# Optimization experiments

Hardware: AMD Instinct MI355X
Metric: run time of the kernel (lower is better)

Reference implementation:

```python
import jax, jax.numpy as jnp
import numpy as np

BNUM, BNOD = 4, 8
NODE_NUM = BNUM * BNUM * BNOD  # 128
EPS = 1e-9


def setup_inputs() -> dict:
    key = jax.random.key(0)
    k1, k2, k3 = jax.random.split(key, 3)
    x = jax.random.normal(k1, (8, 512, 64, 64), dtype=jnp.float32)
    anchor = jax.random.uniform(k2, (NODE_NUM, 512), dtype=jnp.float32)
    sigma = jax.random.uniform(k3, (NODE_NUM, 512), dtype=jnp.float32)
    return {"x": x, "anchor": anchor, "sigma": sigma}


def reference(x, anchor, sigma):
    B, C, H, W = x.shape
    h, w = H // BNUM, W // BNUM
    n = h * w                       # pixels per spatial block
    G = BNUM * BNUM                 # number of spatial blocks
    # Gather all spatial blocks at once: (B,C,H,W) -> (B, G, n, C)
    blocks = x.reshape(B, C, BNUM, h, BNUM, w)
    blocks = blocks.transpose(0, 2, 4, 3, 5, 1).reshape(B, G, n, C)
    a = anchor.reshape(G, BNOD, C)
    s = sigma.reshape(G, BNOD, C)
    # Gaussian residual per (block, node, pixel): (B, G, BNOD, n, C)
    resid = (blocks[:, :, None, :, :] - a[None, :, :, None, :]) / s[None, :, :, None, :]
    # -||residual||^2 / 2 over channels -> (B, G, BNOD, n)
    logits = -0.5 * jnp.sum(resid * resid, axis=-1)
    # Block-wise softmax over the BNOD nodes of each block
    soft = jax.nn.softmax(logits, axis=2)
    # Soft-assignment-weighted mean residual per node: (B, G, BNOD, C)
    nodes = jnp.einsum('bgknc,bgkn->bgkc', resid, soft)
    nodes = nodes / (jnp.sum(soft, axis=3)[..., None] + EPS)
    # Intra-node L2 normalization over channels (F.normalize, dim=2)
    norm = jnp.linalg.norm(nodes, axis=-1, keepdims=True)
    nodes = nodes / jnp.maximum(norm, 1e-12)
    nodes = nodes.reshape(B, NODE_NUM, C).transpose(0, 2, 1)   # (B, C, node_num)
    soft_assign = soft.reshape(B, NODE_NUM, n)                 # (B, node_num, n)
    return nodes, soft_assign
```

## Files before the change

kernel.cpp:

```cpp
#include <hip/hip_runtime.h>


#define NCH 512

typedef __attribute__((address_space(3))) void lds_void_t;
typedef const __attribute__((address_space(1))) void gbl_void_t;

__device__ __forceinline__ void gload_lds16(const float* g, float* l) {
  __builtin_amdgcn_global_load_lds((gbl_void_t*)g, (lds_void_t*)l, 16, 0, 0);
}

struct SharedMain {
  float anc[NCH * 16];
  float chunk[NCH * 16];
  float scratch[8 * 16 * 8];
  float soft[16 * 8];
};

__global__ __launch_bounds__(512, 4)
void gp_main(const float* __restrict__ x,
             const float* __restrict__ anchor,
             const float* __restrict__ sigma,
             float* __restrict__ soft_out,
             float* __restrict__ ws_s1,
             int parts_log2) {
  __shared__ SharedMain sh;
  const int tid = threadIdx.x;

  const int qb   = blockIdx.x;
  const int xcd  = qb & 7;
  const int slot = qb >> 3;
  const int gx   = slot & 3;
  const int Gp   = slot >> 2;
  const int G    = Gp * 8 + xcd;
  const int gy   = G & 3;
  const int tG   = G >> 2;
  const int parts = 1 << parts_log2;
  const int part  = tG & (parts - 1);
  const int b     = tG >> parts_log2;
  const int g     = gy * 4 + gx;
  const int nrows = 16 >> parts_log2;
  const int y0    = gy * 16 + part * nrows;
  const int x0    = gx * 16;
  const float* xb = x + (size_t)b * (NCH * 4096);

  {
    const float* ab = anchor + g * (8 * NCH);
    const float* sb = sigma  + g * (8 * NCH);
#pragma unroll
    for (int e = 0; e < 8; ++e) {
      int idx = e * 512 + tid;
      int k   = idx >> 9;
      int ci  = idx & 511;
      float a = ab[idx];
      float r = 1.0f / sb[idx];
      int sw  = (ci >> 4) & 3;
      int fq0 = (k >> 2) ^ sw;
      int fq1 = (2 + (k >> 2)) ^ sw;
      sh.anc[ci * 16 + (fq0 << 2) + (k & 3)] = r;
      sh.anc[ci * 16 + (fq1 << 2) + (k & 3)] = a * r;
    }
  }

  float S1[8];
#pragma unroll
  for (int k = 0; k < 8; ++k) S1[k] = 0.0f;

  const int cg   = tid >> 4;
  const int p    = tid & 15;
  const int wv   = tid >> 6;
  const int lane = tid & 63;
  const int asw  = cg & 3;

  for (int cc = 0; cc < nrows; ++cc) {
    const int y = y0 + cc;
    __syncthreads();

#pragma unroll
    for (int it = 0; it < 4; ++it) {
      int flat = it * 512 + tid;
      int ci   = flat >> 2;
      int qd   = flat & 3;
      int qs   = qd ^ ((ci >> 1) & 3);
      const float* src = xb + (size_t)ci * 4096 + y * 64 + x0 + (qs << 2);
      gload_lds16(src, &sh.chunk[flat << 2]);
    }
    asm volatile("s_waitcnt vmcnt(0)" ::: "memory");
    __syncthreads();

    float sq[8];
#pragma unroll
    for (int k = 0; k < 8; ++k) sq[k] = 0.0f;
    {
      const float* ancb = sh.anc + cg * 256;
      const int pq = p >> 2, pr = p & 3;
#pragma unroll
      for (int i = 0; i < 16; ++i) {
        const float* ar = ancb + i * 16;
        float4 rlo = *(const float4*)(ar + ((0 ^ asw) << 2));
        float4 rhi = *(const float4*)(ar + ((1 ^ asw) << 2));
        float4 alo = *(const float4*)(ar + ((2 ^ asw) << 2));
        float4 ahi = *(const float4*)(ar + ((3 ^ asw) << 2));
        int ci = (cg << 4) + i;
        float xv = sh.chunk[(ci << 4) + ((pq ^ ((ci >> 1) & 3)) << 2) + pr];
        float t;
        t = fmaf(xv, rlo.x, -alo.x); sq[0] = fmaf(t, t, sq[0]);
        t = fmaf(xv, rlo.y, -alo.y); sq[1] = fmaf(t, t, sq[1]);
        t = fmaf(xv, rlo.z, -alo.z); sq[2] = fmaf(t, t, sq[2]);
        t = fmaf(xv, rlo.w, -alo.w); sq[3] = fmaf(t, t, sq[3]);
        t = fmaf(xv, rhi.x, -ahi.x); sq[4] = fmaf(t, t, sq[4]);
        t = fmaf(xv, rhi.y, -ahi.y); sq[5] = fmaf(t, t, sq[5]);
        t = fmaf(xv, rhi.z, -ahi.z); sq[6] = fmaf(t, t, sq[6]);
        t = fmaf(xv, rhi.w, -ahi.w); sq[7] = fmaf(t, t, sq[7]);
      }
    }
#pragma unroll
    for (int k = 0; k < 8; ++k) {
      sq[k] += __shfl_xor(sq[k], 16, 64);
      sq[k] += __shfl_xor(sq[k], 32, 64);
    }
    if (lane < 16) {
      *(float4*)&sh.scratch[((wv << 4) + lane) << 3]       =
          make_float4(sq[0], sq[1], sq[2], sq[3]);
      *(float4*)&sh.scratch[(((wv << 4) + lane) << 3) + 4] =
          make_float4(sq[4], sq[5], sq[6], sq[7]);
    }
    __syncthreads();

    if (tid < 128) {
      int pp = tid >> 3, k = tid & 7;
      float acc = 0.0f;
#pragma unroll
      for (int w = 0; w < 8; ++w) acc += sh.scratch[((w << 4) + pp) * 8 + k];
      float l = -0.5f * acc;
      float mx = l;
      mx = fmaxf(mx, __shfl_xor(mx, 1, 64));
      mx = fmaxf(mx, __shfl_xor(mx, 2, 64));
      mx = fmaxf(mx, __shfl_xor(mx, 4, 64));
      float e = __expf(l - mx);
      float es = e;
      es += __shfl_xor(es, 1, 64);
      es += __shfl_xor(es, 2, 64);
      es += __shfl_xor(es, 4, 64);
      sh.soft[(pp << 3) + k] = e / es;
    }
    __syncthreads();

    if (tid < 128) {
      int k = tid >> 4, pp = tid & 15;
      soft_out[(size_t)((b << 7) + (g << 3) + k) * 256 +
               (part * nrows + cc) * 16 + pp] = sh.soft[(pp << 3) + k];
    }

    {
      const float* ch = sh.chunk + (tid << 4);
      const int csw = (tid >> 1) & 3;
#pragma unroll
      for (int qd = 0; qd < 4; ++qd) {
        float4 xv = *(const float4*)(ch + ((qd ^ csw) << 2));
#pragma unroll
        for (int j = 0; j < 4; ++j) {
          float xvj = (j == 0) ? xv.x : (j == 1) ? xv.y : (j == 2) ? xv.z : xv.w;
          const float* sp = &sh.soft[((qd << 2) + j) << 3];
          float4 s0 = *(const float4*)sp;
          float4 s1 = *(const float4*)(sp + 4);
          S1[0] = fmaf(xvj, s0.x, S1[0]);
          S1[1] = fmaf(xvj, s0.y, S1[1]);
          S1[2] = fmaf(xvj, s0.z, S1[2]);
          S1[3] = fmaf(xvj, s0.w, S1[3]);
          S1[4] = fmaf(xvj, s1.x, S1[4]);
          S1[5] = fmaf(xvj, s1.y, S1[5]);
          S1[6] = fmaf(xvj, s1.z, S1[6]);
          S1[7] = fmaf(xvj, s1.w, S1[7]);
        }
      }
    }
  }

  const int bg = (b << 4) + g;
  float* wp = ws_s1 + ((size_t)(bg * parts + part) << 3) * NCH + tid;
#pragma unroll
  for (int k = 0; k < 8; ++k) wp[k * NCH] = S1[k];
}

__global__ __launch_bounds__(512, 4)
void gp_final(const float* __restrict__ anchor,
              const float* __restrict__ sigma,
              const float* __restrict__ soft_out,
              const float* __restrict__ ws_s1,
              float* __restrict__ nodes_out,
              int parts) {
  const int bg = blockIdx.x;
  const int b  = bg >> 4, g = bg & 15;
  const int tid = threadIdx.x;
  __shared__ float sS0[8];
  __shared__ float red[8 * 8];
  __shared__ float invn[8];

  if (tid < 256) {
    int k = tid >> 5, sl = tid & 31;
    const float* sp = soft_out + (size_t)((b << 7) + (g << 3) + k) * 256 + (sl << 3);
    float4 a0 = *(const float4*)sp;
    float4 a1 = *(const float4*)(sp + 4);
    float v = a0.x + a0.y + a0.z + a0.w + a1.x + a1.y + a1.z + a1.w;
    v += __shfl_xor(v, 1, 64);
    v += __shfl_xor(v, 2, 64);
    v += __shfl_xor(v, 4, 64);
    v += __shfl_xor(v, 8, 64);
    v += __shfl_xor(v, 16, 64);
    if (sl == 0) sS0[k] = v;
  }
  __syncthreads();

  float S1[8];
#pragma unroll
  for (int k = 0; k < 8; ++k) S1[k] = 0.0f;
  for (int pt = 0; pt < parts; ++pt) {
    const float* wp = ws_s1 + ((size_t)(bg * parts + pt) << 3) * NCH + tid;
#pragma unroll
    for (int k = 0; k < 8; ++k) S1[k] += wp[k * NCH];
  }

  float v[8];
#pragma unroll
  for (int k = 0; k < 8; ++k) {
    float s  = sigma [((g << 3) + k) * NCH + tid];
    float a  = anchor[((g << 3) + k) * NCH + tid];
    float rs = 1.0f / s;
    float S0 = sS0[k];
    float nd = rs * S1[k] - (a * rs) * S0;
    v[k] = nd / (S0 + 1e-9f);
  }

  const int wv = tid >> 6, lane = tid & 63;
#pragma unroll
  for (int k = 0; k < 8; ++k) {
    float s = v[k] * v[k];
    s += __shfl_xor(s, 1, 64);
    s += __shfl_xor(s, 2, 64);
    s += __shfl_xor(s, 4, 64);
    s += __shfl_xor(s, 8, 64);
    s += __shfl_xor(s, 16, 64);
    s += __shfl_xor(s, 32, 64);
    if (lane == 0) red[(wv << 3) + k] = s;
  }
  __syncthreads();
  if (tid < 8) {
    float t2 = 0.0f;
#pragma unroll
    for (int w = 0; w < 8; ++w) t2 += red[(w << 3) + tid];
    invn[tid] = 1.0f / fmaxf(sqrtf(t2), 1e-12f);
  }
  __syncthreads();

  float4 o0 = make_float4(v[0] * invn[0], v[1] * invn[1], v[2] * invn[2], v[3] * invn[3]);
  float4 o1 = make_float4(v[4] * invn[4], v[5] * invn[5], v[6] * invn[6], v[7] * invn[7]);
  float* dst = nodes_out + ((size_t)(b * NCH) + tid) * 128 + (g << 3);
  *(float4*)(dst)     = o0;
  *(float4*)(dst + 4) = o1;
}

extern "C" void kernel_launch(void* const* d_in, const int* in_sizes, int n_in,
                              void* d_out, int out_size, void* d_ws, size_t ws_size,
                              hipStream_t stream) {
  const float* x      = (const float*)d_in[0];
  const float* anchor = (const float*)d_in[1];
  const float* sigma  = (const float*)d_in[2];
  float* out = (float*)d_out;
  float* wsf = (float*)d_ws;

  int parts_log2;
  const size_t need4 = (size_t)128 * 4 * 8 * NCH * sizeof(float);
  if      (ws_size >= need4)     parts_log2 = 2;
  else if (ws_size >= need4 / 2) parts_log2 = 1;
  else                           parts_log2 = 0;
  const int parts = 1 << parts_log2;

  float* soft_out = out + 524288;

  gp_main <<<128 * parts, 512, 0, stream>>>(x, anchor, sigma, soft_out, wsf,
                                            parts_log2);
  gp_final<<<128, 512, 0, stream>>>(anchor, sigma, soft_out, wsf, out, parts);
}
```

Measured before the change: 41.05 us.

## Split fused main kernel into prep, logits, and double-buffered accumulation kernels

Replaces the single fused kernel, which computed logits, softmax and weighted sums row by row behind several barriers, with separate kernels. A prep kernel precomputes 1/sigma and anchor/sigma into workspace. A logits kernel reads x directly from global memory to compute the softmax. An accumulation kernel then re-reads x through double-buffered LDS staging and uses the stored soft assignments. This removes the per-row serialization and the anchor LDS setup in each block, but reads x twice and adds two kernel launches.

```diff
diff --git a/kernel.cpp b/kernel.cpp
--- a/kernel.cpp
+++ b/kernel.cpp
@@ -10,171 +10,174 @@
   __builtin_amdgcn_global_load_lds((gbl_void_t*)g, (lds_void_t*)l, 16, 0, 0);
 }
 
-struct SharedMain {
-  float anc[NCH * 16];
-  float chunk[NCH * 16];
-  float scratch[8 * 16 * 8];
-  float soft[16 * 8];
-};
-
-__global__ __launch_bounds__(512, 4)
-void gp_main(const float* __restrict__ x,
-             const float* __restrict__ anchor,
+__global__ __launch_bounds__(512, 2)
+void gp_prep(const float* __restrict__ anchor,
              const float* __restrict__ sigma,
-             float* __restrict__ soft_out,
-             float* __restrict__ ws_s1,
-             int parts_log2) {
-  __shared__ SharedMain sh;
+             float* __restrict__ ws_anc) {
+  const int g = blockIdx.x;
+  const int c = threadIdx.x;
+  float vals[16];
+#pragma unroll
+  for (int k = 0; k < 8; ++k) {
+    float a = anchor[((g << 3) + k) * NCH + c];
+    float s = sigma [((g << 3) + k) * NCH + c];
+    float r = 1.0f / s;
+    vals[k]     = r;
+    vals[k + 8] = a * r;
+  }
+  float4* dst = (float4*)(ws_anc + (((size_t)g * NCH + c) << 4));
+#pragma unroll
+  for (int q = 0; q < 4; ++q) dst[q] = ((float4*)vals)[q];
+}
+
+__global__ __launch_bounds__(512, 2)
+void gp_logits(const float* __restrict__ x,
+               const float* __restrict__ ws_anc,
+               float* __restrict__ soft_out) {
+  __shared__ float sc[8 * 64 * 8];
   const int tid = threadIdx.x;
-
-  const int qb   = blockIdx.x;
-  const int xcd  = qb & 7;
-  const int slot = qb >> 3;
-  const int gx   = slot & 3;
-  const int Gp   = slot >> 2;
-  const int G    = Gp * 8 + xcd;
-  const int gy   = G & 3;
-  const int tG   = G >> 2;
-  const int parts = 1 << parts_log2;
-  const int part  = tG & (parts - 1);
-  const int b     = tG >> parts_log2;
-  const int g     = gy * 4 + gx;
-  const int nrows = 16 >> parts_log2;
-  const int y0    = gy * 16 + part * nrows;
-  const int x0    = gx * 16;
+  const int bid = blockIdx.x;
+  const int gx = bid >> 7;
+  const int r  = bid & 127;
+  const int q  = r & 3;
+  const int gy = (r >> 2) & 3;
+  const int b  = r >> 4;
+  const int g  = (gy << 2) + gx;
+  const int w  = __builtin_amdgcn_readfirstlane(tid >> 6);
+  const int lane = tid & 63;
+  const int prow = lane >> 4, pcol = lane & 15;
+  const int y = (gy << 4) + (q << 2) + prow;
+
+  const float* xp = x + (size_t)b * (NCH * 4096)
+                      + (size_t)(w << 6) * 4096 + y * 64 + (gx << 4) + pcol;
+  const float4* ap = (const float4*)(ws_anc + (((size_t)g * NCH + (w << 6)) << 4));
+
+  float sq[8];
+#pragma unroll
+  for (int k = 0; k < 8; ++k) sq[k] = 0.0f;
+
+#pragma unroll 8
+  for (int cc = 0; cc < 64; ++cc) {
+    float xv = xp[(size_t)cc * 4096];
+    float4 r0 = ap[(cc << 2) + 0];
+    float4 r1 = ap[(cc << 2) + 1];
+    float4 a0 = ap[(cc << 2) + 2];
+    float4 a1 = ap[(cc << 2) + 3];
+    float t;
+    t = fmaf(xv, r0.x, -a0.x); sq[0] = fmaf(t, t, sq[0]);
+    t = fmaf(xv, r0.y, -a0.y); sq[1] = fmaf(t, t, sq[1]);
+    t = fmaf(xv, r0.z, -a0.z); sq[2] = fmaf(t, t, sq[2]);
+    t = fmaf(xv, r0.w, -a0.w); sq[3] = fmaf(t, t, sq[3]);
+    t = fmaf(xv, r1.x, -a1.x); sq[4] = fmaf(t, t, sq[4]);
+    t = fmaf(xv, r1.y, -a1.y); sq[5] = fmaf(t, t, sq[5]);
+    t = fmaf(xv, r1.z, -a1.z); sq[6] = fmaf(t, t, sq[6]);
+    t = fmaf(xv, r1.w, -a1.w); sq[7] = fmaf(t, t, sq[7]);
+  }
+
+  const int sbase = ((w << 6) + lane) << 3;
+  *(float4*)&sc[sbase]     = make_float4(sq[0], sq[1], sq[2], sq[3]);
+  *(float4*)&sc[sbase + 4] = make_float4(sq[4], sq[5], sq[6], sq[7]);
+  __syncthreads();
+
+  {
+    const int px = tid >> 3, k = tid & 7;
+    float acc = 0.0f;
+#pragma unroll
+    for (int w2 = 0; w2 < 8; ++w2) acc += sc[(w2 << 9) + tid];
+    float l = -0.5f * acc;
+    float mx = l;
+    mx = fmaxf(mx, __shfl_xor(mx, 1, 64));
+    mx = fmaxf(mx, __shfl_xor(mx, 2, 64));
+    mx = fmaxf(mx, __shfl_xor(mx, 4, 64));
+    float e = __expf(l - mx);
+    float es = e;
+    es += __shfl_xor(es, 1, 64);
+    es += __shfl_xor(es, 2, 64);
+    es += __shfl_xor(es, 4, 64);
+    soft_out[(size_t)((b << 7) + (g << 3) + k) * 256 + (q << 6) + px] = e / es;
+  }
+}
+
+__global__ __launch_bounds__(512, 2)
+void gp_accum(const float* __restrict__ x,
+              const float* __restrict__ soft_in,
+              float* __restrict__ ws_s1,
+              int plog) {
+  __shared__ float chunk[2][NCH * 16];
+  __shared__ float soft_lds[256 * 8];
+  const int tid = threadIdx.x;
+  const int bid = blockIdx.x;
+  const int parts = 1 << plog;
+  const int gx = bid >> (5 + plog);
+  const int r  = bid & ((32 << plog) - 1);
+  const int part = r & (parts - 1);
+  const int gy = (r >> plog) & 3;
+  const int b  = r >> (plog + 2);
+  const int g  = (gy << 2) + gx;
+  const int nrows = 16 >> plog;
+  const int npx   = nrows << 4;
+  const int y0 = (gy << 4) + part * nrows;
+  const int x0 = gx << 4;
   const float* xb = x + (size_t)b * (NCH * 4096);
 
-  {
-    const float* ab = anchor + g * (8 * NCH);
-    const float* sb = sigma  + g * (8 * NCH);
-#pragma unroll
-    for (int e = 0; e < 8; ++e) {
-      int idx = e * 512 + tid;
-      int k   = idx >> 9;
-      int ci  = idx & 511;
-      float a = ab[idx];
-      float r = 1.0f / sb[idx];
-      int sw  = (ci >> 4) & 3;
-      int fq0 = (k >> 2) ^ sw;
-      int fq1 = (2 + (k >> 2)) ^ sw;
-      sh.anc[ci * 16 + (fq0 << 2) + (k & 3)] = r;
-      sh.anc[ci * 16 + (fq1 << 2) + (k & 3)] = a * r;
-    }
-  }
-
-  float S1[8];
-#pragma unroll
-  for (int k = 0; k < 8; ++k) S1[k] = 0.0f;
-
-  const int cg   = tid >> 4;
-  const int p    = tid & 15;
-  const int wv   = tid >> 6;
-  const int lane = tid & 63;
-  const int asw  = cg & 3;
-
-  for (int cc = 0; cc < nrows; ++cc) {
-    const int y = y0 + cc;
-    __syncthreads();
-
+  for (int i = tid; i < npx * 8; i += 512) {
+    int k   = i >> (8 - plog);
+    int pxp = i & (npx - 1);
+    soft_lds[(pxp << 3) + k] =
+        soft_in[(size_t)((b << 7) + (g << 3) + k) * 256 + part * npx + pxp];
+  }
+
+  auto stage = [&](int buf, int row) {
 #pragma unroll
     for (int it = 0; it < 4; ++it) {
       int flat = it * 512 + tid;
       int ci   = flat >> 2;
       int qd   = flat & 3;
       int qs   = qd ^ ((ci >> 1) & 3);
-      const float* src = xb + (size_t)ci * 4096 + y * 64 + x0 + (qs << 2);
-      gload_lds16(src, &sh.chunk[flat << 2]);
+      const float* src = xb + (size_t)ci * 4096 + (y0 + row) * 64 + x0 + (qs << 2);
+      gload_lds16(src, &chunk[buf][flat << 2]);
     }
-    asm volatile("s_waitcnt vmcnt(0)" ::: "memory");
-    __syncthreads();
-
-    float sq[8];
-#pragma unroll
-    for (int k = 0; k < 8; ++k) sq[k] = 0.0f;
-    {
-      const float* ancb = sh.anc + cg * 256;
-      const int pq = p >> 2, pr = p & 3;
-#pragma unroll
-      for (int i = 0; i < 16; ++i) {
-        const float* ar = ancb + i * 16;
-        float4 rlo = *(const float4*)(ar + ((0 ^ asw) << 2));
-        float4 rhi = *(const float4*)(ar + ((1 ^ asw) << 2));
-        float4 alo = *(const float4*)(ar + ((2 ^ asw) << 2));
-        float4 ahi = *(const float4*)(ar + ((3 ^ asw) << 2));
-        int ci = (cg << 4) + i;
-        float xv = sh.chunk[(ci << 4) + ((pq ^ ((ci >> 1) & 3)) << 2) + pr];
-        float t;
-        t = fmaf(xv, rlo.x, -alo.x); sq[0] = fmaf(t, t, sq[0]);
-        t = fmaf(xv, rlo.y, -alo.y); sq[1] = fmaf(t, t, sq[1]);
-        t = fmaf(xv, rlo.z, -alo.z); sq[2] = fmaf(t, t, sq[2]);
-        t = fmaf(xv, rlo.w, -alo.w); sq[3] = fmaf(t, t, sq[3]);
-        t = fmaf(xv, rhi.x, -ahi.x); sq[4] = fmaf(t, t, sq[4]);
-        t = fmaf(xv, rhi.y, -ahi.y); sq[5] = fmaf(t, t, sq[5]);
-        t = fmaf(xv, rhi.z, -ahi.z); sq[6] = fmaf(t, t, sq[6]);
-        t = fmaf(xv, rhi.w, -ahi.w); sq[7] = fmaf(t, t, sq[7]);
+  };
+
+  float S1[8];
+#pragma unroll
+  for (int k = 0; k < 8; ++k) S1[k] = 0.0f;
+
+  stage(0, 0);
+  asm volatile("s_waitcnt lgkmcnt(0)" ::: "memory");
+
+  const int csw = (tid >> 1) & 3;
+  for (int rr = 0; rr < nrows; ++rr) {
+    const int cur = rr & 1;
+    if (rr < nrows - 1) {
+      stage(cur ^ 1, rr + 1);
+      asm volatile("s_waitcnt vmcnt(4)" ::: "memory");
+    } else {
+      asm volatile("s_waitcnt vmcnt(0)" ::: "memory");
+    }
+    asm volatile("s_barrier" ::: "memory");
+
+    const float* ch = &chunk[cur][tid << 4];
+#pragma unroll
+    for (int qd = 0; qd < 4; ++qd) {
+      float4 xv = *(const float4*)(ch + ((qd ^ csw) << 2));
+#pragma unroll
+      for (int j = 0; j < 4; ++j) {
+        float xvj = (j == 0) ? xv.x : (j == 1) ? xv.y : (j == 2) ? xv.z : xv.w;
+        const float* sp = &soft_lds[((rr << 4) + (qd << 2) + j) << 3];
+        float4 s0 = *(const float4*)sp;
+        float4 s1 = *(const float4*)(sp + 4);
+        S1[0] = fmaf(xvj, s0.x, S1[0]);
+        S1[1] = fmaf(xvj, s0.y, S1[1]);
+        S1[2] = fmaf(xvj, s0.z, S1[2]);
+        S1[3] = fmaf(xvj, s0.w, S1[3]);
+        S1[4] = fmaf(xvj, s1.x, S1[4]);
+        S1[5] = fmaf(xvj, s1.y, S1[5]);
+        S1[6] = fmaf(xvj, s1.z, S1[6]);
+        S1[7] = fmaf(xvj, s1.w, S1[7]);
       }
     }
-#pragma unroll
-    for (int k = 0; k < 8; ++k) {
-      sq[k] += __shfl_xor(sq[k], 16, 64);
-      sq[k] += __shfl_xor(sq[k], 32, 64);
-    }
-    if (lane < 16) {
-      *(float4*)&sh.scratch[((wv << 4) + lane) << 3]       =
-          make_float4(sq[0], sq[1], sq[2], sq[3]);
-      *(float4*)&sh.scratch[(((wv << 4) + lane) << 3) + 4] =
-          make_float4(sq[4], sq[5], sq[6], sq[7]);
-    }
-    __syncthreads();
-
-    if (tid < 128) {
-      int pp = tid >> 3, k = tid & 7;
-      float acc = 0.0f;
-#pragma unroll
-      for (int w = 0; w < 8; ++w) acc += sh.scratch[((w << 4) + pp) * 8 + k];
-      float l = -0.5f * acc;
-      float mx = l;
-      mx = fmaxf(mx, __shfl_xor(mx, 1, 64));
-      mx = fmaxf(mx, __shfl_xor(mx, 2, 64));
-      mx = fmaxf(mx, __shfl_xor(mx, 4, 64));
-      float e = __expf(l - mx);
-      float es = e;
-      es += __shfl_xor(es, 1, 64);
-      es += __shfl_xor(es, 2, 64);
-      es += __shfl_xor(es, 4, 64);
-      sh.soft[(pp << 3) + k] = e / es;
-    }
-    __syncthreads();
-
-    if (tid < 128) {
-      int k = tid >> 4, pp = tid & 15;
-      soft_out[(size_t)((b << 7) + (g << 3) + k) * 256 +
-               (part * nrows + cc) * 16 + pp] = sh.soft[(pp << 3) + k];
-    }
-
-    {
-      const float* ch = sh.chunk + (tid << 4);
-      const int csw = (tid >> 1) & 3;
-#pragma unroll
-      for (int qd = 0; qd < 4; ++qd) {
-        float4 xv = *(const float4*)(ch + ((qd ^ csw) << 2));
-#pragma unroll
-        for (int j = 0; j < 4; ++j) {
-          float xvj = (j == 0) ? xv.x : (j == 1) ? xv.y : (j == 2) ? xv.z : xv.w;
-          const float* sp = &sh.soft[((qd << 2) + j) << 3];
-          float4 s0 = *(const float4*)sp;
-          float4 s1 = *(const float4*)(sp + 4);
-          S1[0] = fmaf(xvj, s0.x, S1[0]);
-          S1[1] = fmaf(xvj, s0.y, S1[1]);
-          S1[2] = fmaf(xvj, s0.z, S1[2]);
-          S1[3] = fmaf(xvj, s0.w, S1[3]);
-          S1[4] = fmaf(xvj, s1.x, S1[4]);
-          S1[5] = fmaf(xvj, s1.y, S1[5]);
-          S1[6] = fmaf(xvj, s1.z, S1[6]);
-          S1[7] = fmaf(xvj, s1.w, S1[7]);
-        }
-      }
-    }
+    asm volatile("s_barrier" ::: "memory");
   }
 
   const int bg = (b << 4) + g;
@@ -269,16 +272,19 @@
   float* out = (float*)d_out;
   float* wsf = (float*)d_ws;
 
-  int parts_log2;
-  const size_t need4 = (size_t)128 * 4 * 8 * NCH * sizeof(float);
-  if      (ws_size >= need4)     parts_log2 = 2;
-  else if (ws_size >= need4 / 2) parts_log2 = 1;
-  else                           parts_log2 = 0;
-  const int parts = 1 << parts_log2;
-
-  float* soft_out = out + 524288;
-
-  gp_main <<<128 * parts, 512, 0, stream>>>(x, anchor, sigma, soft_out, wsf,
-                                            parts_log2);
-  gp_final<<<128, 512, 0, stream>>>(anchor, sigma, soft_out, wsf, out, parts);
-}
+  const size_t n_nodes = 524288;
+  float* soft_out = out + n_nodes;
+  float* ws_anc = wsf;
+  float* ws_s1  = wsf + 131072;
+
+  int plog;
+  if      (ws_size >= (131072 + 4u * 524288) * sizeof(float)) plog = 2;
+  else if (ws_size >= (131072 + 2u * 524288) * sizeof(float)) plog = 1;
+  else                                                        plog = 0;
+
+  gp_prep  <<<16,           512, 0, stream>>>(anchor, sigma, ws_anc);
+  gp_logits<<<512,          512, 0, stream>>>(x, ws_anc, soft_out);
+  gp_accum <<<128 << plog,  512, 0, stream>>>(x, soft_out, ws_s1, plog);
+  gp_final <<<128,          512, 0, stream>>>(anchor, sigma, soft_out, ws_s1, out,
+                                              1 << plog);
+}
```

Result: slower. 46.62 us (+13.5%).

## Double-buffer x row loads, precompute anchor tables, batch soft-assignment stores

Applied to the files above, without the earlier changes.

Adds a prep kernel that writes reciprocal-sigma and anchor*reciprocal tables to the workspace once. The main kernel then loads these tables into LDS with async global-to-LDS copies instead of recomputing them in every block. The main kernel double-buffers the x row chunks so the next row's load overlaps the current row's compute, and replaces __syncthreads with explicit waitcnt/barrier. Soft-assignment values are collected in LDS and written out in a batch at the end, and parts is fixed at 2, giving 256 blocks. The costs are an extra kernel launch, more LDS per block (occupancy bound drops to 2) and a fixed workspace layout.

```diff
diff --git a/kernel.cpp b/kernel.cpp
--- a/kernel.cpp
+++ b/kernel.cpp
@@ -2,6 +2,8 @@
 
 
 #define NCH 512
+#define PARTS 2
+#define NROWS 8
 
 typedef __attribute__((address_space(3))) void lds_void_t;
 typedef const __attribute__((address_space(1))) void gbl_void_t;
@@ -10,90 +12,104 @@
   __builtin_amdgcn_global_load_lds((gbl_void_t*)g, (lds_void_t*)l, 16, 0, 0);
 }
 
-struct SharedMain {
+__global__ __launch_bounds__(512, 2)
+void gp_prep(const float* __restrict__ anchor,
+             const float* __restrict__ sigma,
+             float* __restrict__ ws_anc) {
+  const int g = blockIdx.x;
+  const int c = threadIdx.x;
+  float vals[16];
+#pragma unroll
+  for (int k = 0; k < 8; ++k) {
+    float a = anchor[((g << 3) + k) * NCH + c];
+    float s = sigma [((g << 3) + k) * NCH + c];
+    float r = 1.0f / s;
+    vals[k]     = r;
+    vals[k + 8] = a * r;
+  }
+  float4* dst = (float4*)(ws_anc + (((size_t)g * NCH + c) << 4));
+#pragma unroll
+  for (int q = 0; q < 4; ++q) dst[q] = ((float4*)vals)[q];
+}
+
+struct SharedFused {
   float anc[NCH * 16];
-  float chunk[NCH * 16];
+  float chunk[2][NCH * 16];
   float scratch[8 * 16 * 8];
   float soft[16 * 8];
+  float soft_all[NROWS * 128];
 };
 
-__global__ __launch_bounds__(512, 4)
-void gp_main(const float* __restrict__ x,
-             const float* __restrict__ anchor,
-             const float* __restrict__ sigma,
-             float* __restrict__ soft_out,
-             float* __restrict__ ws_s1,
-             int parts_log2) {
-  __shared__ SharedMain sh;
+__global__ __launch_bounds__(512, 2)
+void gp_fused(const float* __restrict__ x,
+              const float* __restrict__ ws_anc,
+              float* __restrict__ soft_out,
+              float* __restrict__ ws_s1) {
+  __shared__ SharedFused sh;
   const int tid = threadIdx.x;
-
-  const int qb   = blockIdx.x;
-  const int xcd  = qb & 7;
-  const int slot = qb >> 3;
-  const int gx   = slot & 3;
-  const int Gp   = slot >> 2;
-  const int G    = Gp * 8 + xcd;
-  const int gy   = G & 3;
-  const int tG   = G >> 2;
-  const int parts = 1 << parts_log2;
-  const int part  = tG & (parts - 1);
-  const int b     = tG >> parts_log2;
-  const int g     = gy * 4 + gx;
-  const int nrows = 16 >> parts_log2;
-  const int y0    = gy * 16 + part * nrows;
-  const int x0    = gx * 16;
+  const int bid = blockIdx.x;
+  const int gx   = bid >> 6;
+  const int r    = bid & 63;
+  const int part = r & 1;
+  const int gy   = (r >> 1) & 3;
+  const int b    = r >> 3;
+  const int g    = (gy << 2) + gx;
+  const int y0   = (gy << 4) + part * NROWS;
+  const int x0   = gx << 4;
   const float* xb = x + (size_t)b * (NCH * 4096);
 
   {
-    const float* ab = anchor + g * (8 * NCH);
-    const float* sb = sigma  + g * (8 * NCH);
-#pragma unroll
-    for (int e = 0; e < 8; ++e) {
-      int idx = e * 512 + tid;
-      int k   = idx >> 9;
-      int ci  = idx & 511;
-      float a = ab[idx];
-      float r = 1.0f / sb[idx];
-      int sw  = (ci >> 4) & 3;
-      int fq0 = (k >> 2) ^ sw;
-      int fq1 = (2 + (k >> 2)) ^ sw;
-      sh.anc[ci * 16 + (fq0 << 2) + (k & 3)] = r;
-      sh.anc[ci * 16 + (fq1 << 2) + (k & 3)] = a * r;
-    }
-  }
+    const float* tb = ws_anc + (size_t)g * (NCH * 16);
+#pragma unroll
+    for (int it = 0; it < 4; ++it) {
+      int qf = it * 512 + tid;
+      int c  = qf >> 2;
+      int p  = qf & 3;
+      int ps = p ^ ((c >> 4) & 3);
+      gload_lds16(tb + c * 16 + (ps << 2), &sh.anc[qf << 2]);
+    }
+  }
+
+  auto stage = [&](int buf, int row) {
+#pragma unroll
+    for (int it = 0; it < 4; ++it) {
+      int qf = it * 512 + tid;
+      int ci = qf >> 2;
+      int qd = qf & 3;
+      int qs = qd ^ ((ci >> 1) & 3);
+      gload_lds16(xb + (size_t)ci * 4096 + (y0 + row) * 64 + x0 + (qs << 2),
+                  &sh.chunk[buf][qf << 2]);
+    }
+  };
+  stage(0, 0);
+  asm volatile("s_waitcnt vmcnt(0) lgkmcnt(0)\ns_barrier" ::: "memory");
 
   float S1[8];
 #pragma unroll
   for (int k = 0; k < 8; ++k) S1[k] = 0.0f;
 
-  const int cg   = tid >> 4;
-  const int p    = tid & 15;
-  const int wv   = tid >> 6;
-  const int lane = tid & 63;
-  const int asw  = cg & 3;
-
-  for (int cc = 0; cc < nrows; ++cc) {
-    const int y = y0 + cc;
-    __syncthreads();
-
-#pragma unroll
-    for (int it = 0; it < 4; ++it) {
-      int flat = it * 512 + tid;
-      int ci   = flat >> 2;
-      int qd   = flat & 3;
-      int qs   = qd ^ ((ci >> 1) & 3);
-      const float* src = xb + (size_t)ci * 4096 + y * 64 + x0 + (qs << 2);
-      gload_lds16(src, &sh.chunk[flat << 2]);
-    }
-    asm volatile("s_waitcnt vmcnt(0)" ::: "memory");
-    __syncthreads();
+  const int cg = tid >> 4, px = tid & 15;
+  const int wv = tid >> 6, lane = tid & 63;
+  const int asw = cg & 3;
+  const int pq = px >> 2, pr = px & 3;
+  const int csw2 = (tid >> 1) & 3;
+
+  for (int rr = 0; rr < NROWS; ++rr) {
+    const int cur = rr & 1;
+    if (rr + 1 < NROWS) {
+      stage(cur ^ 1, rr + 1);
+      asm volatile("s_waitcnt vmcnt(4)" ::: "memory");
+    } else {
+      asm volatile("s_waitcnt vmcnt(0)" ::: "memory");
+    }
+    asm volatile("s_barrier" ::: "memory");
 
     float sq[8];
 #pragma unroll
     for (int k = 0; k < 8; ++k) sq[k] = 0.0f;
     {
       const float* ancb = sh.anc + cg * 256;
-      const int pq = p >> 2, pr = p & 3;
+      const float* chb  = sh.chunk[cur] + (cg << 8);
 #pragma unroll
       for (int i = 0; i < 16; ++i) {
         const float* ar = ancb + i * 16;
@@ -101,8 +117,7 @@
         float4 rhi = *(const float4*)(ar + ((1 ^ asw) << 2));
         float4 alo = *(const float4*)(ar + ((2 ^ asw) << 2));
         float4 ahi = *(const float4*)(ar + ((3 ^ asw) << 2));
-        int ci = (cg << 4) + i;
-        float xv = sh.chunk[(ci << 4) + ((pq ^ ((ci >> 1) & 3)) << 2) + pr];
+        float xv = chb[(i << 4) + (((pq ^ ((i >> 1) & 3))) << 2) + pr];
         float t;
         t = fmaf(xv, rlo.x, -alo.x); sq[0] = fmaf(t, t, sq[0]);
         t = fmaf(xv, rlo.y, -alo.y); sq[1] = fmaf(t, t, sq[1]);
@@ -125,13 +140,12 @@
       *(float4*)&sh.scratch[(((wv << 4) + lane) << 3) + 4] =
           make_float4(sq[4], sq[5], sq[6], sq[7]);
     }
-    __syncthreads();
+    asm volatile("s_waitcnt lgkmcnt(0)\ns_barrier" ::: "memory");
 
     if (tid < 128) {
-      int pp = tid >> 3, k = tid & 7;
       float acc = 0.0f;
 #pragma unroll
-      for (int w = 0; w < 8; ++w) acc += sh.scratch[((w << 4) + pp) * 8 + k];
+      for (int w2 = 0; w2 < 8; ++w2) acc += sh.scratch[(w2 << 7) + tid];
       float l = -0.5f * acc;
       float mx = l;
       mx = fmaxf(mx, __shfl_xor(mx, 1, 64));
@@ -142,22 +156,17 @@
       es += __shfl_xor(es, 1, 64);
       es += __shfl_xor(es, 2, 64);
       es += __shfl_xor(es, 4, 64);
-      sh.soft[(pp << 3) + k] = e / es;
-    }
-    __syncthreads();
-
-    if (tid < 128) {
-      int k = tid >> 4, pp = tid & 15;
-      soft_out[(size_t)((b << 7) + (g << 3) + k) * 256 +
-               (part * nrows + cc) * 16 + pp] = sh.soft[(pp << 3) + k];
-    }
+      float sv = e / es;
+      sh.soft[tid] = sv;
+      sh.soft_all[(rr << 7) + tid] = sv;
+    }
+    asm volatile("s_waitcnt lgkmcnt(0)\ns_barrier" ::: "memory");
 
     {
-      const float* ch = sh.chunk + (tid << 4);
-      const int csw = (tid >> 1) & 3;
+      const float* ch = sh.chunk[cur] + (tid << 4);
 #pragma unroll
       for (int qd = 0; qd < 4; ++qd) {
-        float4 xv = *(const float4*)(ch + ((qd ^ csw) << 2));
+        float4 xv = *(const float4*)(ch + ((qd ^ csw2) << 2));
 #pragma unroll
         for (int j = 0; j < 4; ++j) {
           float xvj = (j == 0) ? xv.x : (j == 1) ? xv.y : (j == 2) ? xv.z : xv.w;
@@ -175,12 +184,26 @@
         }
       }
     }
+    asm volatile("s_barrier" ::: "memory");
   }
 
   const int bg = (b << 4) + g;
-  float* wp = ws_s1 + ((size_t)(bg * parts + part) << 3) * NCH + tid;
-#pragma unroll
-  for (int k = 0; k < 8; ++k) wp[k * NCH] = S1[k];
+  {
+    float* wp = ws_s1 + ((size_t)(bg * PARTS + part) << 3) * NCH + tid;
+#pragma unroll
+    for (int k = 0; k < 8; ++k) wp[k * NCH] = S1[k];
+  }
+  {
+    float* so = soft_out + (size_t)((b << 7) + (g << 3)) * 256 + part * 128;
+#pragma unroll
+    for (int it = 0; it < 2; ++it) {
+      int i   = it * 512 + tid;
+      int k   = i >> 7;
+      int gpx = i & 127;
+      so[(size_t)k * 256 + gpx] =
+          sh.soft_all[((gpx >> 4) << 7) + ((gpx & 15) << 3) + k];
+    }
+  }
 }
 
 __global__ __launch_bounds__(512, 4)
@@ -188,8 +211,7 @@
               const float* __restrict__ sigma,
               const float* __restrict__ soft_out,
               const float* __restrict__ ws_s1,
-              float* __restrict__ nodes_out,
-              int parts) {
+              float* __restrict__ nodes_out) {
   const int bg = blockIdx.x;
   const int b  = bg >> 4, g = bg & 15;
   const int tid = threadIdx.x;
@@ -215,8 +237,9 @@
   float S1[8];
 #pragma unroll
   for (int k = 0; k < 8; ++k) S1[k] = 0.0f;
-  for (int pt = 0; pt < parts; ++pt) {
-    const float* wp = ws_s1 + ((size_t)(bg * parts + pt) << 3) * NCH + tid;
+#pragma unroll
+  for (int pt = 0; pt < PARTS; ++pt) {
+    const float* wp = ws_s1 + ((size_t)(bg * PARTS + pt) << 3) * NCH + tid;
 #pragma unroll
     for (int k = 0; k < 8; ++k) S1[k] += wp[k * NCH];
   }
@@ -269,16 +292,12 @@
   float* out = (float*)d_out;
   float* wsf = (float*)d_ws;
 
-  int parts_log2;
-  const size_t need4 = (size_t)128 * 4 * 8 * NCH * sizeof(float);
-  if      (ws_size >= need4)     parts_log2 = 2;
-  else if (ws_size >= need4 / 2) parts_log2 = 1;
-  else                           parts_log2 = 0;
-  const int parts = 1 << parts_log2;
-
-  float* soft_out = out + 524288;
-
-  gp_main <<<128 * parts, 512, 0, stream>>>(x, anchor, sigma, soft_out, wsf,
-                                            parts_log2);
-  gp_final<<<128, 512, 0, stream>>>(anchor, sigma, soft_out, wsf, out, parts);
-}
+  const size_t n_nodes = 524288;
+  float* soft_out = out + n_nodes;
+  float* ws_anc = wsf;
+  float* ws_s1  = wsf + 131072;
+
+  gp_prep <<<16,  512, 0, stream>>>(anchor, sigma, ws_anc);
+  gp_fused<<<256, 512, 0, stream>>>(x, ws_anc, soft_out, ws_s1);
+  gp_final<<<128, 512, 0, stream>>>(anchor, sigma, soft_out, ws_s1, out);
+}
```

Result: slower. 46.27 us (+12.7%).
